# Kernel tuning notes

Hardware: AMD Instinct MI355X
Metric: run time of the kernel (lower is better)

Reference implementation:

```python
import jax, jax.numpy as jnp
import numpy as np

N, B, T, F_IN, H1, H2 = 69, 32, 1024, 8, 32, 16


def cal_adj_norm(adj):
    # adj_norm = D^-1/2 (A + I) D^-1/2
    n = adj.shape[0]
    adj_ = adj + jnp.eye(n, dtype=adj.dtype)
    d = jnp.sum(adj_, axis=1)
    d_is = d ** -0.5
    return adj_ * d_is[:, None] * d_is[None, :]


def setup_inputs() -> dict:
    key = jax.random.key(0)
    k1, k2, k3, k4 = jax.random.split(key, 4)
    x = jax.random.normal(k1, (N, B, T, F_IN), dtype=jnp.float32)
    a = jax.random.uniform(k2, (N, N), dtype=jnp.float32)
    adj = ((a + a.T) > 1.4).astype(jnp.float32)
    W1 = jax.random.normal(k3, (F_IN, H1), dtype=jnp.float32)
    W2 = jax.random.normal(k4, (H1, H2), dtype=jnp.float32)
    return {"x": x, "adj": adj, "W1": W1, "W2": W2}


def reference(x, adj, W1, W2):
    adj_n = cal_adj_norm(adj)                      # [N, N]
    xb = jnp.transpose(x, (1, 2, 0, 3))            # [B, T, N, F_in]
    # layer 1: relu( adj_n @ x @ W1 ), batched over (B, T)
    h = jax.nn.relu(jnp.einsum('nm,btmf->btnf', adj_n, xb) @ W1)   # [B, T, N, H1]
    # layer 2: sigmoid( adj_n @ h @ W2 )
    out = jax.nn.sigmoid(jnp.einsum('nm,btmf->btnf', adj_n, h) @ W2)  # [B, T, N, H2]
    return out
```

## Files before the change

kernel.cpp:

```cpp
#include <hip/hip_runtime.h>
#include <math.h>

#define N_NODES 69
#define MP      80
#define KP      96
#define BT_TOTAL 32768
#define F_IN    8
#define H1      32
#define H2      16

#define TBT     8
#define BLOCK   256

#define ZPITCH3 104
#define HBPITCH 40

typedef __attribute__((ext_vector_type(8))) short bf16x8;
typedef __attribute__((ext_vector_type(4))) float f32x4;
typedef __attribute__((ext_vector_type(2), aligned(8)))  unsigned u32x2;
typedef __attribute__((ext_vector_type(4), aligned(16))) unsigned u32x4;

typedef bf16x8 __attribute__((may_alias)) bf16x8_a;
typedef u32x2  __attribute__((may_alias)) u32x2_a;
typedef u32x4  __attribute__((may_alias)) u32x4_a;

__device__ __forceinline__ unsigned short f2bf(float f) {
    unsigned u = __float_as_uint(f);
    return (unsigned short)((u + 0x7FFFu + ((u >> 16) & 1u)) >> 16);
}
__device__ __forceinline__ float bf2f(unsigned short h) {
    return __uint_as_float(((unsigned)h) << 16);
}

__global__ void setup_kernel(const float* __restrict__ adj,
                             unsigned short* __restrict__ adjh,
                             unsigned short* __restrict__ adjl)
{
    __shared__ float dinv[N_NODES];
    const int tid = threadIdx.x;
    if (tid < N_NODES) {
        float s = 1.0f;
        for (int j = 0; j < N_NODES; ++j) s += adj[tid * N_NODES + j];
        dinv[tid] = rsqrtf(s);
    }
    __syncthreads();
    for (int idx = tid; idx < MP * KP; idx += BLOCK) {
        const int n = idx / KP, m = idx % KP;
        float v = 0.0f;
        if (n < N_NODES && m < N_NODES) {
            float a = adj[n * N_NODES + m] + (n == m ? 1.0f : 0.0f);
            v = a * dinv[n] * dinv[m];
        }
        unsigned short h = f2bf(v);
        adjh[idx] = h;
        adjl[idx] = f2bf(v - bf2f(h));
    }
}

__global__ __launch_bounds__(BLOCK, 4) void gcn_kernel(
    const float* __restrict__ x,
    const unsigned short* __restrict__ adjh,
    const unsigned short* __restrict__ adjl,
    const float* __restrict__ W1g,
    const float* __restrict__ W2g,
    float* __restrict__ out)
{
    __shared__ unsigned short Zt[128 * ZPITCH3];
    __shared__ unsigned short Hb_s[4][2][16 * HBPITCH];

    const int tid  = threadIdx.x;
    const int lane = tid & 63;
    const int wv   = tid >> 6;
    const int quad = lane >> 4;
    const int l16  = lane & 15;
    const int bt0  = blockIdx.x * TBT;

    {
        const int row = wv * 32 + (lane >> 1);
        const int col = 80 + (lane & 1) * 8;
        *(u32x4_a*)&Zt[row * ZPITCH3 + col] = (u32x4){0u, 0u, 0u, 0u};
    }

    bf16x8 ahf[15];
#pragma unroll
    for (int t = 0; t < 15; ++t) {
        const int nt = t / 3, kt = t % 3;
        ahf[t] = *(const bf16x8_a*)&adjh[(nt * 16 + l16) * KP + kt * 32 + quad * 8];
    }

    const int btg = bt0 + wv * 2 + (l16 >> 3);
    const int fl  = l16 & 7;

    float xv[3][8];
#pragma unroll
    for (int kt = 0; kt < 3; ++kt) {
#pragma unroll
        for (int p = 0; p < 4; ++p) {
            const int m0 = kt * 32 + quad * 8 + 2 * p;
            const int m1 = m0 + 1;
            if (kt < 2) {
                xv[kt][2 * p]     = x[(size_t)m0 * 262144 + btg * 8 + fl];
                xv[kt][2 * p + 1] = x[(size_t)m1 * 262144 + btg * 8 + fl];
            } else {
                xv[kt][2 * p]     = (m0 < N_NODES) ? x[(size_t)m0 * 262144 + btg * 8 + fl] : 0.0f;
                xv[kt][2 * p + 1] = (m1 < N_NODES) ? x[(size_t)m1 * 262144 + btg * 8 + fl] : 0.0f;
            }
        }
    }

    f32x4 acc[5] = {};
#pragma unroll
    for (int kt = 0; kt < 3; ++kt) {
        union AF { unsigned u[4]; bf16x8 v; } ah, al;
#pragma unroll
        for (int p = 0; p < 4; ++p) {
            const float x0 = xv[kt][2 * p], x1 = xv[kt][2 * p + 1];
            const unsigned short h0 = f2bf(x0), h1 = f2bf(x1);
            ah.u[p] = (unsigned)h0 | ((unsigned)h1 << 16);
            const unsigned short g0 = f2bf(x0 - bf2f(h0));
            const unsigned short g1 = f2bf(x1 - bf2f(h1));
            al.u[p] = (unsigned)g0 | ((unsigned)g1 << 16);
        }
        bf16x8 alf[5];
#pragma unroll
        for (int nt = 0; nt < 5; ++nt)
            alf[nt] = *(const bf16x8_a*)&adjl[(nt * 16 + l16) * KP + kt * 32 + quad * 8];
#pragma unroll
        for (int nt = 0; nt < 5; ++nt) {
            acc[nt] = __builtin_amdgcn_mfma_f32_16x16x32_bf16(ah.v, ahf[nt * 3 + kt], acc[nt], 0, 0, 0);
            acc[nt] = __builtin_amdgcn_mfma_f32_16x16x32_bf16(ah.v, alf[nt], acc[nt], 0, 0, 0);
            acc[nt] = __builtin_amdgcn_mfma_f32_16x16x32_bf16(al.v, ahf[nt * 3 + kt], acc[nt], 0, 0, 0);
        }
    }

    bf16x8 w1f[2][2] = {};
    {
        const int fb0 = quad * 4;
        const int fb1 = (quad - 2) * 4;
#pragma unroll
        for (int ht = 0; ht < 2; ++ht) {
#pragma unroll
            for (int j = 0; j < 4; ++j) {
                const float a0 = (quad < 2)  ? W1g[(fb0 + j) * H1 + ht * 16 + l16] : 0.0f;
                const float a1 = (quad >= 2) ? W1g[(fb1 + j) * H1 + ht * 16 + l16] : 0.0f;
                w1f[0][ht][j] = (short)f2bf(a0);
                w1f[1][ht][j] = (short)f2bf(a1);
            }
        }
    }
    bf16x8 w2f;
#pragma unroll
    for (int j = 0; j < 8; ++j)
        w2f[j] = (short)f2bf(W2g[(quad * 8 + j) * H2 + l16]);

    auto do_bt = [&](const f32x4& h0, const f32x4& h1, int btl, int nt,
                     unsigned short* Hb) {
#pragma unroll
        for (int reg = 0; reg < 4; ++reg) {
            const int row = quad * 4 + reg;
            Hb[row * HBPITCH + l16]      = f2bf(fmaxf(h0[reg], 0.f));
            Hb[row * HBPITCH + 16 + l16] = f2bf(fmaxf(h1[reg], 0.f));
        }
        const bf16x8 a2 = *(const bf16x8_a*)&Hb[l16 * HBPITCH + quad * 8];
        f32x4 zk = {0.f, 0.f, 0.f, 0.f};
        zk = __builtin_amdgcn_mfma_f32_16x16x32_bf16(a2, w2f, zk, 0, 0, 0);
        const unsigned z0 = (unsigned)f2bf(zk[0]) | ((unsigned)f2bf(zk[1]) << 16);
        const unsigned z1 = (unsigned)f2bf(zk[2]) | ((unsigned)f2bf(zk[3]) << 16);
        *(u32x2_a*)&Zt[(btl * 16 + l16) * ZPITCH3 + nt * 16 + quad * 4] = (u32x2){z0, z1};
    };

#pragma unroll
    for (int nt = 0; nt < 5; ++nt) {
        const unsigned d0 = (unsigned)f2bf(acc[nt][0]) | ((unsigned)f2bf(acc[nt][1]) << 16);
        const unsigned d1 = (unsigned)f2bf(acc[nt][2]) | ((unsigned)f2bf(acc[nt][3]) << 16);
        union AF { unsigned u[4]; bf16x8 v; } af;
        af.u[0] = d0; af.u[1] = d1; af.u[2] = d0; af.u[3] = d1;

        const f32x4 zz = {0.f, 0.f, 0.f, 0.f};
        f32x4 hL0 = __builtin_amdgcn_mfma_f32_16x16x32_bf16(af.v, w1f[0][0], zz, 0, 0, 0);
        f32x4 hL1 = __builtin_amdgcn_mfma_f32_16x16x32_bf16(af.v, w1f[0][1], zz, 0, 0, 0);
        f32x4 hH0 = __builtin_amdgcn_mfma_f32_16x16x32_bf16(af.v, w1f[1][0], zz, 0, 0, 0);
        f32x4 hH1 = __builtin_amdgcn_mfma_f32_16x16x32_bf16(af.v, w1f[1][1], zz, 0, 0, 0);

        do_bt(hL0, hL1, wv * 2 + 0, nt, &Hb_s[wv][0][0]);
        do_bt(hH0, hH1, wv * 2 + 1, nt, &Hb_s[wv][1][0]);
    }

    __syncthreads();

    bf16x8 bz[2][3];
#pragma unroll
    for (int c = 0; c < 2; ++c)
#pragma unroll
        for (int kt = 0; kt < 3; ++kt)
            bz[c][kt] = *(const bf16x8_a*)
                &Zt[((wv * 2 + c) * 16 + l16) * ZPITCH3 + kt * 32 + quad * 8];

#pragma unroll
    for (int mt = 0; mt < 5; ++mt) {
#pragma unroll
        for (int c = 0; c < 2; ++c) {
            f32x4 a3 = {0.f, 0.f, 0.f, 0.f};
#pragma unroll
            for (int kt = 0; kt < 3; ++kt)
                a3 = __builtin_amdgcn_mfma_f32_16x16x32_bf16(ahf[mt * 3 + kt], bz[c][kt], a3, 0, 0, 0);
            const int ct3 = wv * 2 + c;
            float* outc = out + ((size_t)(bt0 + ct3) * N_NODES) * H2 + l16;
#pragma unroll
            for (int reg = 0; reg < 4; ++reg) {
                const int n = mt * 16 + quad * 4 + reg;
                if (n < N_NODES) {
                    const float v = 1.0f / (1.0f + __expf(-a3[reg]));
                    outc[n * H2] = v;
                }
            }
        }
    }
}

extern "C" void kernel_launch(void* const* d_in, const int* in_sizes, int n_in,
                              void* d_out, int out_size, void* d_ws, size_t ws_size,
                              hipStream_t stream) {
    const float* x   = (const float*)d_in[0];
    const float* adj = (const float*)d_in[1];
    const float* W1  = (const float*)d_in[2];
    const float* W2  = (const float*)d_in[3];
    float* out = (float*)d_out;

    unsigned short* adjh = (unsigned short*)d_ws;
    unsigned short* adjl = adjh + MP * KP;

    setup_kernel<<<1, BLOCK, 0, stream>>>(adj, adjh, adjl);
    gcn_kernel<<<BT_TOTAL / TBT, BLOCK, 0, stream>>>(x, adjh, adjl, W1, W2, out);
}
```

Measured before the change: 259.2 us.

## Process four bt-groups per block with register-prefetched x across groups

Each block now loops over four consecutive groups of eight (b,t) slices, so the grid shrinks to a quarter and the W1/W2 fragment setup is amortized across groups. The x loads for the next group are issued after the current group's layer-1 MFMAs, which double-buffers x in registers and overlaps global latency with the layer-1 epilogue and layer-2 compute. The 15 adjacency-high fragments are no longer held in registers; they are re-read from global/L1 where needed, cutting register pressure but adding cached loads. The risk is fewer blocks for latency hiding and extra load traffic for adjacency fragments.

Result: slower. 309.5 us (+19.4%).

```diff
diff --git a/kernel.cpp b/kernel.cpp
--- a/kernel.cpp
+++ b/kernel.cpp
@@ -10,7 +10,9 @@
 #define H2      16
 
 #define TBT     8
+#define NGROUPS 4
 #define BLOCK   256
+#define GRID    (BT_TOTAL / (TBT * NGROUPS))
 
 #define ZPITCH3 104
 #define HBPITCH 40
@@ -73,64 +75,12 @@
     const int wv   = tid >> 6;
     const int quad = lane >> 4;
     const int l16  = lane & 15;
-    const int bt0  = blockIdx.x * TBT;
+    const int fl   = l16 & 7;
 
     {
         const int row = wv * 32 + (lane >> 1);
         const int col = 80 + (lane & 1) * 8;
         *(u32x4_a*)&Zt[row * ZPITCH3 + col] = (u32x4){0u, 0u, 0u, 0u};
-    }
-
-    bf16x8 ahf[15];
-#pragma unroll
-    for (int t = 0; t < 15; ++t) {
-        const int nt = t / 3, kt = t % 3;
-        ahf[t] = *(const bf16x8_a*)&adjh[(nt * 16 + l16) * KP + kt * 32 + quad * 8];
-    }
-
-    const int btg = bt0 + wv * 2 + (l16 >> 3);
-    const int fl  = l16 & 7;
-
-    float xv[3][8];
-#pragma unroll
-    for (int kt = 0; kt < 3; ++kt) {
-#pragma unroll
-        for (int p = 0; p < 4; ++p) {
-            const int m0 = kt * 32 + quad * 8 + 2 * p;
-            const int m1 = m0 + 1;
-            if (kt < 2) {
-                xv[kt][2 * p]     = x[(size_t)m0 * 262144 + btg * 8 + fl];
-                xv[kt][2 * p + 1] = x[(size_t)m1 * 262144 + btg * 8 + fl];
-            } else {
-                xv[kt][2 * p]     = (m0 < N_NODES) ? x[(size_t)m0 * 262144 + btg * 8 + fl] : 0.0f;
-                xv[kt][2 * p + 1] = (m1 < N_NODES) ? x[(size_t)m1 * 262144 + btg * 8 + fl] : 0.0f;
-            }
-        }
-    }
-
-    f32x4 acc[5] = {};
-#pragma unroll
-    for (int kt = 0; kt < 3; ++kt) {
-        union AF { unsigned u[4]; bf16x8 v; } ah, al;
-#pragma unroll
-        for (int p = 0; p < 4; ++p) {
-            const float x0 = xv[kt][2 * p], x1 = xv[kt][2 * p + 1];
-            const unsigned short h0 = f2bf(x0), h1 = f2bf(x1);
-            ah.u[p] = (unsigned)h0 | ((unsigned)h1 << 16);
-            const unsigned short g0 = f2bf(x0 - bf2f(h0));
-            const unsigned short g1 = f2bf(x1 - bf2f(h1));
-            al.u[p] = (unsigned)g0 | ((unsigned)g1 << 16);
-        }
-        bf16x8 alf[5];
-#pragma unroll
-        for (int nt = 0; nt < 5; ++nt)
-            alf[nt] = *(const bf16x8_a*)&adjl[(nt * 16 + l16) * KP + kt * 32 + quad * 8];
-#pragma unroll
-        for (int nt = 0; nt < 5; ++nt) {
-            acc[nt] = __builtin_amdgcn_mfma_f32_16x16x32_bf16(ah.v, ahf[nt * 3 + kt], acc[nt], 0, 0, 0);
-            acc[nt] = __builtin_amdgcn_mfma_f32_16x16x32_bf16(ah.v, alf[nt], acc[nt], 0, 0, 0);
-            acc[nt] = __builtin_amdgcn_mfma_f32_16x16x32_bf16(al.v, ahf[nt * 3 + kt], acc[nt], 0, 0, 0);
-        }
     }
 
     bf16x8 w1f[2][2] = {};
@@ -153,69 +103,132 @@
     for (int j = 0; j < 8; ++j)
         w2f[j] = (short)f2bf(W2g[(quad * 8 + j) * H2 + l16]);
 
-    auto do_bt = [&](const f32x4& h0, const f32x4& h1, int btl, int nt,
-                     unsigned short* Hb) {
-#pragma unroll
-        for (int reg = 0; reg < 4; ++reg) {
-            const int row = quad * 4 + reg;
-            Hb[row * HBPITCH + l16]      = f2bf(fmaxf(h0[reg], 0.f));
-            Hb[row * HBPITCH + 16 + l16] = f2bf(fmaxf(h1[reg], 0.f));
-        }
-        const bf16x8 a2 = *(const bf16x8_a*)&Hb[l16 * HBPITCH + quad * 8];
-        f32x4 zk = {0.f, 0.f, 0.f, 0.f};
-        zk = __builtin_amdgcn_mfma_f32_16x16x32_bf16(a2, w2f, zk, 0, 0, 0);
-        const unsigned z0 = (unsigned)f2bf(zk[0]) | ((unsigned)f2bf(zk[1]) << 16);
-        const unsigned z1 = (unsigned)f2bf(zk[2]) | ((unsigned)f2bf(zk[3]) << 16);
-        *(u32x2_a*)&Zt[(btl * 16 + l16) * ZPITCH3 + nt * 16 + quad * 4] = (u32x2){z0, z1};
+    auto loadX = [&](float (&xv)[3][8], int bt0g) {
+        const int btg = bt0g + wv * 2 + (l16 >> 3);
+#pragma unroll
+        for (int kt = 0; kt < 3; ++kt) {
+#pragma unroll
+            for (int p = 0; p < 4; ++p) {
+                const int m0 = kt * 32 + quad * 8 + 2 * p;
+                const int m1 = m0 + 1;
+                if (kt < 2) {
+                    xv[kt][2 * p]     = x[(size_t)m0 * 262144 + btg * 8 + fl];
+                    xv[kt][2 * p + 1] = x[(size_t)m1 * 262144 + btg * 8 + fl];
+                } else {
+                    xv[kt][2 * p]     = (m0 < N_NODES) ? x[(size_t)m0 * 262144 + btg * 8 + fl] : 0.0f;
+                    xv[kt][2 * p + 1] = (m1 < N_NODES) ? x[(size_t)m1 * 262144 + btg * 8 + fl] : 0.0f;
+                }
+            }
+        }
     };
 
-#pragma unroll
-    for (int nt = 0; nt < 5; ++nt) {
-        const unsigned d0 = (unsigned)f2bf(acc[nt][0]) | ((unsigned)f2bf(acc[nt][1]) << 16);
-        const unsigned d1 = (unsigned)f2bf(acc[nt][2]) | ((unsigned)f2bf(acc[nt][3]) << 16);
-        union AF { unsigned u[4]; bf16x8 v; } af;
-        af.u[0] = d0; af.u[1] = d1; af.u[2] = d0; af.u[3] = d1;
-
-        const f32x4 zz = {0.f, 0.f, 0.f, 0.f};
-        f32x4 hL0 = __builtin_amdgcn_mfma_f32_16x16x32_bf16(af.v, w1f[0][0], zz, 0, 0, 0);
-        f32x4 hL1 = __builtin_amdgcn_mfma_f32_16x16x32_bf16(af.v, w1f[0][1], zz, 0, 0, 0);
-        f32x4 hH0 = __builtin_amdgcn_mfma_f32_16x16x32_bf16(af.v, w1f[1][0], zz, 0, 0, 0);
-        f32x4 hH1 = __builtin_amdgcn_mfma_f32_16x16x32_bf16(af.v, w1f[1][1], zz, 0, 0, 0);
-
-        do_bt(hL0, hL1, wv * 2 + 0, nt, &Hb_s[wv][0][0]);
-        do_bt(hH0, hH1, wv * 2 + 1, nt, &Hb_s[wv][1][0]);
-    }
-
-    __syncthreads();
-
-    bf16x8 bz[2][3];
-#pragma unroll
-    for (int c = 0; c < 2; ++c)
-#pragma unroll
-        for (int kt = 0; kt < 3; ++kt)
-            bz[c][kt] = *(const bf16x8_a*)
-                &Zt[((wv * 2 + c) * 16 + l16) * ZPITCH3 + kt * 32 + quad * 8];
-
-#pragma unroll
-    for (int mt = 0; mt < 5; ++mt) {
-#pragma unroll
-        for (int c = 0; c < 2; ++c) {
-            f32x4 a3 = {0.f, 0.f, 0.f, 0.f};
+    auto body = [&](float (&xc)[3][8], float (&xn)[3][8], int bt0g, bool pref) {
+        f32x4 acc[5] = {};
+#pragma unroll
+        for (int kt = 0; kt < 3; ++kt) {
+            union AF { unsigned u[4]; bf16x8 v; } ah, al;
+#pragma unroll
+            for (int p = 0; p < 4; ++p) {
+                const float x0 = xc[kt][2 * p], x1 = xc[kt][2 * p + 1];
+                const unsigned short h0 = f2bf(x0), h1 = f2bf(x1);
+                ah.u[p] = (unsigned)h0 | ((unsigned)h1 << 16);
+                const unsigned short g0 = f2bf(x0 - bf2f(h0));
+                const unsigned short g1 = f2bf(x1 - bf2f(h1));
+                al.u[p] = (unsigned)g0 | ((unsigned)g1 << 16);
+            }
+            bf16x8 bhf[5], blf[5];
+#pragma unroll
+            for (int nt = 0; nt < 5; ++nt) {
+                const int boff = (nt * 16 + l16) * KP + kt * 32 + quad * 8;
+                bhf[nt] = *(const bf16x8_a*)&adjh[boff];
+                blf[nt] = *(const bf16x8_a*)&adjl[boff];
+            }
+#pragma unroll
+            for (int nt = 0; nt < 5; ++nt) {
+                acc[nt] = __builtin_amdgcn_mfma_f32_16x16x32_bf16(ah.v, bhf[nt], acc[nt], 0, 0, 0);
+                acc[nt] = __builtin_amdgcn_mfma_f32_16x16x32_bf16(ah.v, blf[nt], acc[nt], 0, 0, 0);
+                acc[nt] = __builtin_amdgcn_mfma_f32_16x16x32_bf16(al.v, bhf[nt], acc[nt], 0, 0, 0);
+            }
+        }
+
+        if (pref) loadX(xn, bt0g + TBT);
+
+        auto do_bt = [&](const f32x4& h0, const f32x4& h1, int btl, int nt,
+                         unsigned short* Hb) {
+#pragma unroll
+            for (int reg = 0; reg < 4; ++reg) {
+                const int row = quad * 4 + reg;
+                Hb[row * HBPITCH + l16]      = f2bf(fmaxf(h0[reg], 0.f));
+                Hb[row * HBPITCH + 16 + l16] = f2bf(fmaxf(h1[reg], 0.f));
+            }
+            const bf16x8 a2 = *(const bf16x8_a*)&Hb[l16 * HBPITCH + quad * 8];
+            f32x4 zk = {0.f, 0.f, 0.f, 0.f};
+            zk = __builtin_amdgcn_mfma_f32_16x16x32_bf16(a2, w2f, zk, 0, 0, 0);
+            const unsigned z0 = (unsigned)f2bf(zk[0]) | ((unsigned)f2bf(zk[1]) << 16);
+            const unsigned z1 = (unsigned)f2bf(zk[2]) | ((unsigned)f2bf(zk[3]) << 16);
+            *(u32x2_a*)&Zt[(btl * 16 + l16) * ZPITCH3 + nt * 16 + quad * 4] = (u32x2){z0, z1};
+        };
+
+#pragma unroll
+        for (int nt = 0; nt < 5; ++nt) {
+            const unsigned d0 = (unsigned)f2bf(acc[nt][0]) | ((unsigned)f2bf(acc[nt][1]) << 16);
+            const unsigned d1 = (unsigned)f2bf(acc[nt][2]) | ((unsigned)f2bf(acc[nt][3]) << 16);
+            union AF { unsigned u[4]; bf16x8 v; } af;
+            af.u[0] = d0; af.u[1] = d1; af.u[2] = d0; af.u[3] = d1;
+
+            const f32x4 zz = {0.f, 0.f, 0.f, 0.f};
+            f32x4 hL0 = __builtin_amdgcn_mfma_f32_16x16x32_bf16(af.v, w1f[0][0], zz, 0, 0, 0);
+            f32x4 hL1 = __builtin_amdgcn_mfma_f32_16x16x32_bf16(af.v, w1f[0][1], zz, 0, 0, 0);
+            f32x4 hH0 = __builtin_amdgcn_mfma_f32_16x16x32_bf16(af.v, w1f[1][0], zz, 0, 0, 0);
+            f32x4 hH1 = __builtin_amdgcn_mfma_f32_16x16x32_bf16(af.v, w1f[1][1], zz, 0, 0, 0);
+
+            do_bt(hL0, hL1, wv * 2 + 0, nt, &Hb_s[wv][0][0]);
+            do_bt(hH0, hH1, wv * 2 + 1, nt, &Hb_s[wv][1][0]);
+        }
+
+        __syncthreads();
+
+        bf16x8 bz[2][3];
+#pragma unroll
+        for (int c = 0; c < 2; ++c)
 #pragma unroll
             for (int kt = 0; kt < 3; ++kt)
-                a3 = __builtin_amdgcn_mfma_f32_16x16x32_bf16(ahf[mt * 3 + kt], bz[c][kt], a3, 0, 0, 0);
-            const int ct3 = wv * 2 + c;
-            float* outc = out + ((size_t)(bt0 + ct3) * N_NODES) * H2 + l16;
-#pragma unroll
-            for (int reg = 0; reg < 4; ++reg) {
-                const int n = mt * 16 + quad * 4 + reg;
-                if (n < N_NODES) {
-                    const float v = 1.0f / (1.0f + __expf(-a3[reg]));
-                    outc[n * H2] = v;
+                bz[c][kt] = *(const bf16x8_a*)
+                    &Zt[((wv * 2 + c) * 16 + l16) * ZPITCH3 + kt * 32 + quad * 8];
+
+#pragma unroll
+        for (int mt = 0; mt < 5; ++mt) {
+            bf16x8 am[3];
+#pragma unroll
+            for (int kt = 0; kt < 3; ++kt)
+                am[kt] = *(const bf16x8_a*)&adjh[(mt * 16 + l16) * KP + kt * 32 + quad * 8];
+#pragma unroll
+            for (int c = 0; c < 2; ++c) {
+                f32x4 a3 = {0.f, 0.f, 0.f, 0.f};
+#pragma unroll
+                for (int kt = 0; kt < 3; ++kt)
+                    a3 = __builtin_amdgcn_mfma_f32_16x16x32_bf16(am[kt], bz[c][kt], a3, 0, 0, 0);
+                const int ct3 = wv * 2 + c;
+                float* outc = out + ((size_t)(bt0g + ct3) * N_NODES) * H2 + l16;
+#pragma unroll
+                for (int reg = 0; reg < 4; ++reg) {
+                    const int n = mt * 16 + quad * 4 + reg;
+                    if (n < N_NODES) {
+                        const float v = 1.0f / (1.0f + __expf(-a3[reg]));
+                        outc[n * H2] = v;
+                    }
                 }
             }
         }
-    }
+    };
+
+    const int bt0 = blockIdx.x * (TBT * NGROUPS);
+    float xvA[3][8], xvB[3][8];
+    loadX(xvA, bt0);
+    body(xvA, xvB, bt0 + 0 * TBT, true);
+    body(xvB, xvA, bt0 + 1 * TBT, true);
+    body(xvA, xvB, bt0 + 2 * TBT, true);
+    body(xvB, xvA, bt0 + 3 * TBT, false);
 }
 
 extern "C" void kernel_launch(void* const* d_in, const int* in_sizes, int n_in,
@@ -231,5 +244,5 @@
     unsigned short* adjl = adjh + MP * KP;
 
     setup_kernel<<<1, BLOCK, 0, stream>>>(adj, adjh, adjl);
-    gcn_kernel<<<BT_TOTAL / TBT, BLOCK, 0, stream>>>(x, adjh, adjl, W1, W2, out);
-}
+    gcn_kernel<<<GRID, BLOCK, 0, stream>>>(x, adjh, adjl, W1, W2, out);
+}
```
